# Kernel optimization log

Hardware: AMD Instinct MI355X
Metric: run time of the kernel (lower is better)

Reference implementation:

```python
import jax, jax.numpy as jnp
import numpy as np

N_GENE, N_DRUG, N_CLASS, N_FAM = 100000, 50000, 2000, 5000
D = 64
E_CG, E_CP, E_GF = 2000000, 100000, 200000
N_PAIRS = 100000


def setup_inputs() -> dict:
    key = jax.random.key(0)
    ks = jax.random.split(key, 32)
    nrm = lambda k, s, sc=0.1: jax.random.normal(k, s, jnp.float32) * sc
    ri = lambda k, n, hi: jax.random.randint(k, (n,), 0, hi, jnp.int32)
    inp = {
        "gene_emb": nrm(ks[0], (N_GENE, D)),
        "drug_emb": nrm(ks[1], (N_DRUG, D)),
        "class_emb": nrm(ks[2], (N_CLASS, D)),
        "family_emb": nrm(ks[3], (N_FAM, D)),
        "W_msg": nrm(ks[4], (2, 6, D, D)),
        "b_msg": jnp.zeros((2, 6, D), jnp.float32),
        "W_root": nrm(ks[5], (2, 6, D, D)),
        "Wc1": nrm(ks[6], (2 * D, D)),
        "bc1": jnp.zeros((D,), jnp.float32),
        "Wc2": nrm(ks[7], (D, 4)),
        "bc2": jnp.zeros((4,), jnp.float32),
        "e_cg_src": ri(ks[8], E_CG, N_DRUG), "e_cg_dst": ri(ks[9], E_CG, N_GENE),
        "e_gc_src": ri(ks[10], E_CG, N_GENE), "e_gc_dst": ri(ks[11], E_CG, N_DRUG),
        "e_cp_src": ri(ks[12], E_CP, N_DRUG), "e_cp_dst": ri(ks[13], E_CP, N_CLASS),
        "e_pc_src": ri(ks[14], E_CP, N_CLASS), "e_pc_dst": ri(ks[15], E_CP, N_DRUG),
        "e_gf_src": ri(ks[16], E_GF, N_GENE), "e_gf_dst": ri(ks[17], E_GF, N_FAM),
        "e_fg_src": ri(ks[18], E_GF, N_FAM), "e_fg_dst": ri(ks[19], E_GF, N_GENE),
        "pair_drug": ri(ks[20], N_PAIRS, N_DRUG),
        "pair_gene": ri(ks[21], N_PAIRS, N_GENE),
    }
    return inp


def _sage(x_src, x_dst, src, dst, n_dst, Wm, bm, Wr):
    # PyG SAGEConv(aggr='mean'): lin_l(mean_j x_src[j]) + lin_r(x_dst)
    msg = x_src[src]                                            # [E, D] gather
    agg = jax.ops.segment_sum(msg, dst, num_segments=n_dst)     # [n_dst, D]
    cnt = jax.ops.segment_sum(jnp.ones(src.shape, msg.dtype), dst, num_segments=n_dst)
    mean = agg / jnp.maximum(cnt, 1.0)[:, None]                 # isolated nodes -> 0
    return mean @ Wm + bm + x_dst @ Wr


def reference(gene_emb, drug_emb, class_emb, family_emb, W_msg, b_msg, W_root,
              Wc1, bc1, Wc2, bc2,
              e_cg_src, e_cg_dst, e_gc_src, e_gc_dst, e_cp_src, e_cp_dst,
              e_pc_src, e_pc_dst, e_gf_src, e_gf_dst, e_fg_src, e_fg_dst,
              pair_drug, pair_gene):
    sizes = {"gene": N_GENE, "compound": N_DRUG, "pclass": N_CLASS, "family": N_FAM}
    rels = [  # (src_type, dst_type, src_idx, dst_idx), order matches W_msg relation axis
        ("compound", "gene", e_cg_src, e_cg_dst),
        ("gene", "compound", e_gc_src, e_gc_dst),
        ("compound", "pclass", e_cp_src, e_cp_dst),
        ("pclass", "compound", e_pc_src, e_pc_dst),
        ("gene", "family", e_gf_src, e_gf_dst),
        ("family", "gene", e_fg_src, e_fg_dst),
    ]
    x = {"gene": gene_emb, "compound": drug_emb, "pclass": class_emb, "family": family_emb}
    num_layers = 2
    for l in range(num_layers):
        out = {k: jnp.zeros((sizes[k], D), jnp.float32) for k in sizes}  # HeteroConv aggr='sum'
        for r, (s, d, src, dst) in enumerate(rels):
            out[d] = out[d] + _sage(x[s], x[d], src, dst, sizes[d],
                                    W_msg[l, r], b_msg[l, r], W_root[l, r])
        x = out
        if l < num_layers - 1:
            x = {k: jax.nn.relu(v) for k, v in x.items()}  # dropout = identity (eval)
    h = jnp.concatenate([x["compound"][pair_drug], x["gene"][pair_gene]], axis=-1)  # [N, 2D]
    h = jax.nn.relu(h @ Wc1 + bc1)
    return h @ Wc2 + bc2  # [N, 4]
```

## Files before the change

kernel.cpp:

```cpp
#include <hip/hip_runtime.h>
#include <hip/hip_bf16.h>

#define NG 100000
#define ND 50000
#define NC 2000
#define NF 5000
#define DD 64

#define BSH 9
#define BINW 512
#define NREL 6
#define NB_CG ((NG + BINW - 1) / BINW)
#define NB_GC ((ND + BINW - 1) / BINW)
#define NB_CP ((NC + BINW - 1) / BINW)
#define NB_PC ((ND + BINW - 1) / BINW)
#define NB_GF ((NF + BINW - 1) / BINW)
#define NB_FG ((NG + BINW - 1) / BINW)
#define TOTB (NB_CG + NB_GC + NB_CP + NB_PC + NB_GF + NB_FG)
#define CHUNK 4096

typedef _Float16 h2_t __attribute__((ext_vector_type(2)));
typedef _Float16 half8 __attribute__((ext_vector_type(8)));
typedef float f32x4 __attribute__((ext_vector_type(4)));

__device__ inline uint packh2_rne(float a, float b) {
    h2_t h; h.x = (_Float16)a; h.y = (_Float16)b;
    return __builtin_bit_cast(uint, h);
}
__device__ inline float2 h2f2(uint u) {
    h2_t h = __builtin_bit_cast(h2_t, u);
    return make_float2((float)h.x, (float)h.y);
}
__device__ inline float fdot2u(uint m, uint w, float acc) {
#if __has_builtin(__builtin_amdgcn_fdot2)
    return __builtin_amdgcn_fdot2(__builtin_bit_cast(h2_t, m),
                                  __builtin_bit_cast(h2_t, w), acc, false);
#else
    float2 a = h2f2(m), b = h2f2(w);
    return acc + a.x * b.x + a.y * b.y;
#endif
}

struct Cvt4 { const float* in[4]; uint* out[4]; int n2[4]; };
struct EdgeJobs {
    const int* src[NREL]; const int* dst[NREL];
    int binbase[NREL]; int E[NREL]; int blk_end[NREL];
};
struct BPackJobs {
    const float* A[6]; const float* B[6]; const float* Ra[6]; const float* Rb[6];
    uint4* out[6]; int nkt[6];
};

struct MegaA {
    EdgeJobs ej; Cvt4 cv; BPackJobs bp;
    const float* Wc1; uint2* pwWc1;
    int hist_blocks, cvt_blocks;
    int* ghist;
};
__global__ __launch_bounds__(256) void megaA_kernel(MegaA a) {
    int b = blockIdx.x;
    if (b < a.hist_blocks) {
        __shared__ int lh[TOTB];
        for (int t = threadIdx.x; t < TOTB; t += 256) lh[t] = 0;
        __syncthreads();
        int j = 0;
        while (b >= a.ej.blk_end[j]) ++j;
        int b0 = j ? a.ej.blk_end[j - 1] : 0;
        int e0 = (b - b0) * CHUNK;
        const int* dst = a.ej.dst[j];
        int E = a.ej.E[j], bb = a.ej.binbase[j];
        for (int t = threadIdx.x; t < CHUNK; t += 256) {
            int e = e0 + t;
            if (e < E) atomicAdd(&lh[bb + (dst[e] >> BSH)], 1);
        }
        __syncthreads();
        for (int t = threadIdx.x; t < TOTB; t += 256)
            if (lh[t]) atomicAdd(&a.ghist[t], lh[t]);
    } else if (b < a.hist_blocks + a.cvt_blocks) {
        int cb = b - a.hist_blocks;
        for (int j = 0; j < 4; ++j) {
            int n2 = a.cv.n2[j];
            const float2* ip = (const float2*)a.cv.in[j];
            uint* op = a.cv.out[j];
            for (int i = cb * 256 + threadIdx.x; i < n2; i += a.cvt_blocks * 256)
                op[i] = packh2_rne(ip[i].x, ip[i].y);
        }
    } else if (b == a.hist_blocks + a.cvt_blocks) {
        const float* A = a.Wc1;
        uint2* o = a.pwWc1;
        for (int t = threadIdx.x; t < 32 * 64; t += 256) {
            int k4 = t >> 6, c = t & 63;
            float v0 = A[(4 * k4 + 0) * 64 + c];
            float v1 = A[(4 * k4 + 1) * 64 + c];
            float v2 = A[(4 * k4 + 2) * 64 + c];
            float v3 = A[(4 * k4 + 3) * 64 + c];
            o[t] = make_uint2(packh2_rne(v0, v1), packh2_rne(v2, v3));
        }
    } else {
        int pj = b - a.hist_blocks - a.cvt_blocks - 1;
        const float* A = a.bp.A[pj];
        const float* B = a.bp.B[pj];
        const float* Ra = a.bp.Ra[pj];
        const float* Rb = a.bp.Rb[pj];
        uint4* o = a.bp.out[pj];
        int n = a.bp.nkt[pj] * 4 * 64;
        for (int t = threadIdx.x; t < n; t += 256) {
            int kt = t >> 8, nt = (t >> 6) & 3, l = t & 63;
            int col = nt * 16 + (l & 15);
            float v[8];
#pragma unroll
            for (int j = 0; j < 8; ++j) {
                int k = kt * 32 + ((l >> 4) << 3) + j;
                int sel = k >> 6, r = k & 63;
                float x;
                if (sel == 0) x = A[r * 64 + col];
                else if (sel == 1 && B) x = B[r * 64 + col];
                else x = Ra[r * 64 + col] + (Rb ? Rb[r * 64 + col] : 0.f);
                v[j] = x;
            }
            o[t] = make_uint4(packh2_rne(v[0], v[1]), packh2_rne(v[2], v[3]),
                              packh2_rne(v[4], v[5]), packh2_rne(v[6], v[7]));
        }
    }
}

__global__ void scanB_kernel(const int* __restrict__ ghist, int* __restrict__ gbinstart,
                             int* __restrict__ gcursor) {
    int lane = threadIdx.x;
    if (lane >= 64) return;
    int carry = 0;
    for (int base = 0; base < TOTB; base += 64) {
        int idx = base + lane;
        int v = (idx < TOTB) ? ghist[idx] : 0;
        int ts = v;
        for (int d = 1; d < 64; d <<= 1) { int t = __shfl_up(ts, d); if (lane >= d) ts += t; }
        int excl = carry + ts - v;
        if (idx < TOTB) { gbinstart[idx] = excl; gcursor[idx] = excl; }
        carry += __shfl(ts, 63);
    }
    if (lane == 0) gbinstart[TOTB] = carry;
}

__global__ __launch_bounds__(256) void scatC_kernel(EdgeJobs ej, int* __restrict__ gcursor,
                                                    int* __restrict__ binned) {
    __shared__ int lh[TOTB], lbase[TOTB];
    for (int t = threadIdx.x; t < TOTB; t += 256) lh[t] = 0;
    __syncthreads();
    int b = blockIdx.x, j = 0;
    while (b >= ej.blk_end[j]) ++j;
    int b0 = j ? ej.blk_end[j - 1] : 0;
    int e0 = (b - b0) * CHUNK;
    const int* dst = ej.dst[j];
    const int* srcp = ej.src[j];
    int E = ej.E[j], bb = ej.binbase[j];
    for (int t = threadIdx.x; t < CHUNK; t += 256) {
        int e = e0 + t;
        if (e < E) atomicAdd(&lh[bb + (dst[e] >> BSH)], 1);
    }
    __syncthreads();
    for (int t = threadIdx.x; t < TOTB; t += 256) {
        int c = lh[t];
        if (c) { lbase[t] = atomicAdd(&gcursor[t], c); lh[t] = 0; }
    }
    __syncthreads();
    for (int t = threadIdx.x; t < CHUNK; t += 256) {
        int e = e0 + t;
        if (e < E) {
            int d = dst[e];
            int bin = bb + (d >> BSH);
            int p = atomicAdd(&lh[bin], 1);
            binned[lbase[bin] + p] = (srcp[e] << BSH) | (d & (BINW - 1));
        }
    }
}

struct BinMeta { int relbase[NREL + 1]; int* off[NREL]; int ndst[NREL]; };
__global__ __launch_bounds__(256) void csrD_kernel(BinMeta bmt, const int* __restrict__ gbinstart,
                                                   const int* __restrict__ binned,
                                                   int* __restrict__ adj) {
    __shared__ int lcnt[BINW], lexc[BINW];
    int b = blockIdx.x, j = 0;
    while (b >= bmt.relbase[j + 1]) ++j;
    int lb = b - bmt.relbase[j];
    int n0 = lb << BSH;
    int nn = bmt.ndst[j] - n0; if (nn > BINW) nn = BINW;
    int es = gbinstart[b], ee = gbinstart[b + 1];
    for (int t = threadIdx.x; t < BINW; t += 256) lcnt[t] = 0;
    __syncthreads();
    for (int t = es + threadIdx.x; t < ee; t += 256)
        atomicAdd(&lcnt[binned[t] & (BINW - 1)], 1);
    __syncthreads();
    if (threadIdx.x < 64) {
        int lane = threadIdx.x, carry = 0;
        for (int base = 0; base < BINW; base += 64) {
            int v = lcnt[base + lane];
            int ts = v;
            for (int d = 1; d < 64; d <<= 1) { int t2 = __shfl_up(ts, d); if (lane >= d) ts += t2; }
            lexc[base + lane] = carry + ts - v;
            carry += __shfl(ts, 63);
        }
    }
    __syncthreads();
    int* off = bmt.off[j];
    for (int t = threadIdx.x; t < nn; t += 256) off[n0 + t] = es + lexc[t];
    if (threadIdx.x == 0 && n0 + nn == bmt.ndst[j]) off[bmt.ndst[j]] = ee;
    for (int t = threadIdx.x; t < BINW; t += 256) lcnt[t] = 0;
    __syncthreads();
    for (int t = es + threadIdx.x; t < ee; t += 256) {
        int v = binned[t];
        int dl = v & (BINW - 1);
        int p = atomicAdd(&lcnt[dl], 1);
        adj[es + lexc[dl] + p] = v >> BSH;
    }
}

struct GJob { const int* off; const uint4* x; uint4* cat; int cstr, colbase, n, mode; };
struct GatherJobs { GJob jb[6]; int blk_end[6]; };

__global__ __launch_bounds__(256) void gather_kernel(GatherJobs g, const int* __restrict__ adj) {
    int b = blockIdx.x, j = 0;
    while (b >= g.blk_end[j]) ++j;
    int b0 = j ? g.blk_end[j - 1] : 0;
    int nbk = g.blk_end[j] - b0;
    GJob jb = g.jb[j];
    int tid = threadIdx.x, w = tid >> 6, lane = tid & 63;
    int cq = lane & 7, rg = lane >> 3;
    if (jb.mode == 0) {
        int side = rg >> 2, sub = rg & 3;
        int npair = (jb.n + 1) >> 1;
        for (int p = (b - b0) * 4 + w; p < npair; p += nbk * 4) {
            int ia = p * 2;
            bool hb = (ia + 1 < jb.n);
            int a0 = jb.off[ia], a1 = jb.off[ia + 1];
            int b1 = hb ? jb.off[ia + 2] : a1;
            int cnt = side ? (b1 - a1) : (a1 - a0);
            const int* base = adj + (side ? a1 : a0);
            half8 acc = {0, 0, 0, 0, 0, 0, 0, 0};
            int full = cnt & ~3;
            for (int e = sub; e < full; e += 4) {
                int idx = base[e];
                acc += *(const half8*)(jb.x + (long long)idx * 8 + cq);
            }
            int e = full + sub;
            if (e < cnt) {
                int idx = base[e];
                acc += *(const half8*)(jb.x + (long long)idx * 8 + cq);
            }
            uint4 u = __builtin_bit_cast(uint4, acc), o;
            o.x = __shfl_xor((int)u.x, 8); o.y = __shfl_xor((int)u.y, 8);
            o.z = __shfl_xor((int)u.z, 8); o.w = __shfl_xor((int)u.w, 8);
            acc += __builtin_bit_cast(half8, o);
            u = __builtin_bit_cast(uint4, acc);
            o.x = __shfl_xor((int)u.x, 16); o.y = __shfl_xor((int)u.y, 16);
            o.z = __shfl_xor((int)u.z, 16); o.w = __shfl_xor((int)u.w, 16);
            acc += __builtin_bit_cast(half8, o);
            float invf = 1.f / fmaxf((float)cnt, 1.f);
            _Float16 ih = (_Float16)invf;
            half8 iv = {ih, ih, ih, ih, ih, ih, ih, ih};
            acc *= iv;
            if (sub == 0 && (side == 0 || hb)) {
                int node = ia + side;
                jb.cat[(long long)node * jb.cstr + jb.colbase + cq] =
                    __builtin_bit_cast(uint4, acc);
            }
        }
    } else {
        for (int gp = (b - b0) * 4 + w; gp * 8 < jb.n; gp += nbk * 4) {
            int node = gp * 8 + rg;
            int nc = node < jb.n ? node : jb.n - 1;
            int o0 = jb.off[nc], o1 = jb.off[nc + 1];
            int cnt = (node < jb.n) ? (o1 - o0) : 0;
            half8 acc = {0, 0, 0, 0, 0, 0, 0, 0};
            for (int t = 0; t < cnt; ++t) {
                int idx = adj[o0 + t];
                acc += *(const half8*)(jb.x + (long long)idx * 8 + cq);
            }
            float invf = 1.f / fmaxf((float)cnt, 1.f);
            _Float16 ih = (_Float16)invf;
            half8 iv = {ih, ih, ih, ih, ih, ih, ih, ih};
            acc *= iv;
            if (node < jb.n)
                jb.cat[(long long)node * jb.cstr + jb.colbase + cq] =
                    __builtin_bit_cast(uint4, acc);
        }
    }
}

struct ApplyJobs {
    const uint4* cat[4]; const uint4* xr[4]; const uint4* Bimg[4];
    const float* bA[4]; const float* bB[4];
    ushort* out[4];
    int cat_kt[4]; int cstr4[4]; int n[4]; int relu[4]; int blk_end[4];
};
__global__ __launch_bounds__(256) void apply_kernel(ApplyJobs a, int njobs) {
    int b = blockIdx.x, j = 0;
    while (b >= a.blk_end[j]) ++j;
    int b0 = j ? a.blk_end[j - 1] : 0;
    int jb = a.blk_end[j] - b0;
    int n = a.n[j], cat_kt = a.cat_kt[j], cstr4 = a.cstr4[j], relu = a.relu[j];
    int K_kt = cat_kt + 2;
    const uint4* cat = a.cat[j];
    const uint4* xr = a.xr[j];
    const uint4* Bimg = a.Bimg[j];
    const float* bA = a.bA[j];
    const float* bB = a.bB[j];
    ushort* out = a.out[j];
    int tid = threadIdx.x;
    int w = tid >> 6, lane = tid & 63;
    int mrow = lane & 15, koct = lane >> 4;
    int tiles = (n + 15) >> 4;
    for (int t = (b - b0) * 4 + w; t < tiles; t += jb * 4) {
        int m0 = t << 4;
        int row = m0 + mrow;
        if (row > n - 1) row = n - 1;
        f32x4 acc0 = {0.f, 0.f, 0.f, 0.f};
        f32x4 acc1 = {0.f, 0.f, 0.f, 0.f};
        f32x4 acc2 = {0.f, 0.f, 0.f, 0.f};
        f32x4 acc3 = {0.f, 0.f, 0.f, 0.f};
        for (int kt = 0; kt < K_kt; ++kt) {
            uint4 av;
            if (kt < cat_kt) av = cat[(long long)row * cstr4 + kt * 4 + koct];
            else av = xr[(long long)row * 8 + (kt - cat_kt) * 4 + koct];
            half8 af = __builtin_bit_cast(half8, av);
            const uint4* bp = Bimg + kt * 256 + lane;
            half8 b0f = __builtin_bit_cast(half8, bp[0]);
            half8 b1f = __builtin_bit_cast(half8, bp[64]);
            half8 b2f = __builtin_bit_cast(half8, bp[128]);
            half8 b3f = __builtin_bit_cast(half8, bp[192]);
            acc0 = __builtin_amdgcn_mfma_f32_16x16x32_f16(af, b0f, acc0, 0, 0, 0);
            acc1 = __builtin_amdgcn_mfma_f32_16x16x32_f16(af, b1f, acc1, 0, 0, 0);
            acc2 = __builtin_amdgcn_mfma_f32_16x16x32_f16(af, b2f, acc2, 0, 0, 0);
            acc3 = __builtin_amdgcn_mfma_f32_16x16x32_f16(af, b3f, acc3, 0, 0, 0);
        }
        int c = lane & 15, r0 = m0 + (lane >> 4) * 4;
        f32x4 accs[4] = {acc0, acc1, acc2, acc3};
#pragma unroll
        for (int nt = 0; nt < 4; ++nt) {
            int col = nt * 16 + c;
            float bias = bA[col] + (bB ? bB[col] : 0.f);
#pragma unroll
            for (int r = 0; r < 4; ++r) {
                int rw = r0 + r;
                if (rw < n) {
                    float v = accs[nt][r] + bias;
                    if (relu) v = fmaxf(v, 0.f);
                    out[(long long)rw * 64 + col] = __builtin_bit_cast(ushort, (_Float16)v);
                }
            }
        }
    }
}

__global__ __launch_bounds__(256) void classifier_kernel(
        const ushort* __restrict__ xc, const ushort* __restrict__ xg,
        const int* __restrict__ pd, const int* __restrict__ pg,
        const uint2* __restrict__ gW1, const float* __restrict__ bc1,
        const float* __restrict__ Wc2, const float* __restrict__ bc2,
        float* __restrict__ out, int n) {
    __shared__ uint2 sW1[2048];
    __shared__ float sW2[256];
    __shared__ uint2 shp[4][32];
    __shared__ float sh1[4][65];
    int tid = threadIdx.x;
    for (int t = tid; t < 2048; t += 256) sW1[t] = gW1[t];
    if (tid < 256) sW2[tid] = Wc2[tid];
    __syncthreads();
    int lane = tid & 63, sub = tid >> 6;
    float b1 = bc1[lane];
    const uint* xcp = (const uint*)xc;
    const uint* xgp = (const uint*)xg;
    for (int base = blockIdx.x * 4; base < n; base += gridDim.x * 4) {
        int p = base + sub;
        if (p >= n) continue;
        int dp = pd[p], gp = pg[p];
        uint v = (lane < 32) ? xcp[(long long)dp * 32 + lane]
                             : xgp[(long long)gp * 32 + (lane - 32)];
        ((uint*)&shp[sub][0])[lane] = v;
        float acc = b1;
#pragma unroll
        for (int k4 = 0; k4 < 32; ++k4) {
            uint2 wv = sW1[k4 * 64 + lane];
            uint2 mv = shp[sub][k4];
            acc = fdot2u(mv.x, wv.x, acc);
            acc = fdot2u(mv.y, wv.y, acc);
        }
        sh1[sub][lane] = fmaxf(acc, 0.f);
        if (lane < 4) {
            float a2 = bc2[lane];
#pragma unroll 16
            for (int k = 0; k < 64; ++k) a2 += sh1[sub][k] * sW2[k * 4 + lane];
            out[(long long)p * 4 + lane] = a2;
        }
    }
}

extern "C" void kernel_launch(void* const* d_in, const int* in_sizes, int n_in,
                              void* d_out, int out_size, void* d_ws, size_t ws_size,
                              hipStream_t stream) {
    const float* gene = (const float*)d_in[0];
    const float* drug = (const float*)d_in[1];
    const float* pcls = (const float*)d_in[2];
    const float* famb = (const float*)d_in[3];
    const float* Wm   = (const float*)d_in[4];
    const float* bm   = (const float*)d_in[5];
    const float* Wr   = (const float*)d_in[6];
    const float* Wc1  = (const float*)d_in[7];
    const float* bc1  = (const float*)d_in[8];
    const float* Wc2  = (const float*)d_in[9];
    const float* bc2  = (const float*)d_in[10];
    const int* ecg_s = (const int*)d_in[11];
    const int* ecg_d = (const int*)d_in[12];
    const int* egc_s = (const int*)d_in[13];
    const int* egc_d = (const int*)d_in[14];
    const int* ecp_s = (const int*)d_in[15];
    const int* ecp_d = (const int*)d_in[16];
    const int* epc_s = (const int*)d_in[17];
    const int* epc_d = (const int*)d_in[18];
    const int* egf_s = (const int*)d_in[19];
    const int* egf_d = (const int*)d_in[20];
    const int* efg_s = (const int*)d_in[21];
    const int* efg_d = (const int*)d_in[22];
    const int* pair_d = (const int*)d_in[23];
    const int* pair_g = (const int*)d_in[24];
    const int E_CG = in_sizes[11];
    const int E_CP = in_sizes[15];
    const int E_GF = in_sizes[19];
    const int N_PAIRS = in_sizes[23];
    const long long TOT_E = 2LL * E_CG + 2LL * E_CP + 2LL * E_GF;

    ushort* g16   = (ushort*)d_ws;
    ushort* d16   = g16   + (long long)NG * DD;
    ushort* p16   = d16   + (long long)ND * DD;
    ushort* f16b  = p16   + (long long)NC * DD;
    ushort* x1g16 = f16b  + (long long)NF * DD;
    ushort* x1c16 = x1g16 + (long long)NG * DD;
    ushort* x1p16 = x1c16 + (long long)ND * DD;
    ushort* x1f16 = x1p16 + (long long)NC * DD;
    ushort* x2g16 = g16;
    ushort* x2c16 = d16;
    uint2* pwWc1 = (uint2*)(x1f16 + (long long)NF * DD);
    uint4* bimg = (uint4*)(pwWc1 + 2048);
    int* ghist = (int*)(bimg + 6 * 1536);
    int* gbinstart = ghist + TOTB;
    int* gcursor = gbinstart + TOTB + 1;
    int* off_cg = gcursor + TOTB;
    int* off_gc = off_cg + NG + 1;
    int* off_cp = off_gc + ND + 1;
    int* off_pc = off_cp + NC + 1;
    int* off_gf = off_pc + ND + 1;
    int* off_fg = off_gf + NF + 1;
    long long binned_off = (long long)(off_fg + NG + 1 - (int*)d_ws);
    binned_off = (binned_off + 3) & ~3LL;
    int* binned = (int*)d_ws + binned_off;
    int* adj    = binned + TOT_E;
    uint4* cat_c = (uint4*)binned;
    uint4* cat_p = cat_c + (long long)ND * 16;
    uint4* cat_f = cat_p + (long long)NC * 8;
    uint4* cat_g = (uint4*)(adj + TOT_E);

    auto WmLR = [&](int l, int r) { return Wm + (long long)(l * 6 + r) * DD * DD; };
    auto WrLR = [&](int l, int r) { return Wr + (long long)(l * 6 + r) * DD * DD; };
    auto bmLR = [&](int l, int r) { return bm + (long long)(l * 6 + r) * DD; };

    EdgeJobs ej;
    const int* srcs[NREL] = {ecg_s, egc_s, ecp_s, epc_s, egf_s, efg_s};
    const int* dsts[NREL] = {ecg_d, egc_d, ecp_d, epc_d, egf_d, efg_d};
    int Es[NREL] = {E_CG, E_CG, E_CP, E_CP, E_GF, E_GF};
    int bb[NREL] = {0, NB_CG, NB_CG + NB_GC, NB_CG + NB_GC + NB_CP,
                    NB_CG + NB_GC + NB_CP + NB_PC, NB_CG + NB_GC + NB_CP + NB_PC + NB_GF};
    int acc_blocks = 0;
    for (int j = 0; j < NREL; ++j) {
        ej.src[j] = srcs[j]; ej.dst[j] = dsts[j];
        ej.E[j] = Es[j]; ej.binbase[j] = bb[j];
        acc_blocks += (Es[j] + CHUNK - 1) / CHUNK;
        ej.blk_end[j] = acc_blocks;
    }
    const int THIST = acc_blocks;
    const int CVTB = 1024;

    hipMemsetAsync(ghist, 0, TOTB * sizeof(int), stream);
    MegaA ma;
    ma.ej = ej;
    ma.cv.in[0] = gene; ma.cv.out[0] = (uint*)g16;  ma.cv.n2[0] = NG * DD / 2;
    ma.cv.in[1] = drug; ma.cv.out[1] = (uint*)d16;  ma.cv.n2[1] = ND * DD / 2;
    ma.cv.in[2] = pcls; ma.cv.out[2] = (uint*)p16;  ma.cv.n2[2] = NC * DD / 2;
    ma.cv.in[3] = famb; ma.cv.out[3] = (uint*)f16b; ma.cv.n2[3] = NF * DD / 2;
    ma.Wc1 = Wc1; ma.pwWc1 = pwWc1;
    auto setbp = [&](int j, const float* A, const float* B, const float* Ra, const float* Rb, int nkt) {
        ma.bp.A[j] = A; ma.bp.B[j] = B; ma.bp.Ra[j] = Ra; ma.bp.Rb[j] = Rb;
        ma.bp.out[j] = bimg + j * 1536; ma.bp.nkt[j] = nkt;
    };
    setbp(0, WmLR(0, 0), WmLR(0, 5), WrLR(0, 0), WrLR(0, 5), 6);
    setbp(1, WmLR(0, 1), WmLR(0, 3), WrLR(0, 1), WrLR(0, 3), 6);
    setbp(2, WmLR(0, 2), nullptr,    WrLR(0, 2), nullptr,    4);
    setbp(3, WmLR(0, 4), nullptr,    WrLR(0, 4), nullptr,    4);
    setbp(4, WmLR(1, 0), WmLR(1, 5), WrLR(1, 0), WrLR(1, 5), 6);
    setbp(5, WmLR(1, 1), WmLR(1, 3), WrLR(1, 1), WrLR(1, 3), 6);
    ma.hist_blocks = THIST; ma.cvt_blocks = CVTB;
    ma.ghist = ghist;
    megaA_kernel<<<THIST + CVTB + 1 + 6, 256, 0, stream>>>(ma);

    scanB_kernel<<<1, 64, 0, stream>>>(ghist, gbinstart, gcursor);
    scatC_kernel<<<THIST, 256, 0, stream>>>(ej, gcursor, binned);
    BinMeta bmt;
    int rb[NREL + 1] = {0, NB_CG, NB_CG + NB_GC, NB_CG + NB_GC + NB_CP,
                        NB_CG + NB_GC + NB_CP + NB_PC,
                        NB_CG + NB_GC + NB_CP + NB_PC + NB_GF, TOTB};
    int* offs[NREL] = {off_cg, off_gc, off_cp, off_pc, off_gf, off_fg};
    int nds[NREL] = {NG, ND, NC, ND, NF, NG};
    for (int j = 0; j <= NREL; ++j) bmt.relbase[j] = rb[j];
    for (int j = 0; j < NREL; ++j) { bmt.off[j] = offs[j]; bmt.ndst[j] = nds[j]; }
    csrD_kernel<<<TOTB, 256, 0, stream>>>(bmt, gbinstart, binned, adj);

    auto ablk = [](int n) { int b = ((n + 15) / 16 + 3) / 4; return b > 1024 ? 1024 : b; };
    auto gb = [](int E) { int b = E / 1024; if (b < 8) b = 8; if (b > 2048) b = 2048; return b; };

    {
        GatherJobs g;
        int acc = 0;
        auto setg = [&](int j, const int* off, const ushort* x, uint4* cat,
                        int cstr, int colbase, int n, int mode, int E) {
            g.jb[j].off = off; g.jb[j].x = (const uint4*)x; g.jb[j].cat = cat;
            g.jb[j].cstr = cstr; g.jb[j].colbase = colbase; g.jb[j].n = n; g.jb[j].mode = mode;
            acc += gb(E); g.blk_end[j] = acc;
        };
        setg(0, off_cg, d16,  cat_g, 16, 0, NG, 0, E_CG);
        setg(1, off_fg, f16b, cat_g, 16, 8, NG, 1, E_GF);
        setg(2, off_gc, g16,  cat_c, 16, 0, ND, 0, E_CG);
        setg(3, off_pc, p16,  cat_c, 16, 8, ND, 1, E_CP);
        setg(4, off_cp, d16,  cat_p, 8, 0, NC, 0, E_CP);
        setg(5, off_gf, g16,  cat_f, 8, 0, NF, 0, E_GF);
        gather_kernel<<<acc, 256, 0, stream>>>(g, adj);

        ApplyJobs ap;
        auto seta = [&](int j, const uint4* cat, int ckt, int cstr4, const ushort* xr,
                        const uint4* Bi, const float* biA, const float* biB,
                        ushort* out, int n, int relu) {
            ap.cat[j] = cat; ap.cat_kt[j] = ckt; ap.cstr4[j] = cstr4;
            ap.xr[j] = (const uint4*)xr; ap.Bimg[j] = Bi; ap.bA[j] = biA; ap.bB[j] = biB;
            ap.out[j] = out; ap.n[j] = n; ap.relu[j] = relu;
        };
        seta(0, cat_g, 4, 16, g16,  bimg + 0 * 1536, bmLR(0, 0), bmLR(0, 5), x1g16, NG, 1);
        seta(1, cat_c, 4, 16, d16,  bimg + 1 * 1536, bmLR(0, 1), bmLR(0, 3), x1c16, ND, 1);
        seta(2, cat_p, 2, 8,  p16,  bimg + 2 * 1536, bmLR(0, 2), nullptr,    x1p16, NC, 1);
        seta(3, cat_f, 2, 8,  f16b, bimg + 3 * 1536, bmLR(0, 4), nullptr,    x1f16, NF, 1);
        int acc2 = 0;
        for (int j = 0; j < 4; ++j) { acc2 += ablk(ap.n[j]); ap.blk_end[j] = acc2; }
        apply_kernel<<<acc2, 256, 0, stream>>>(ap, 4);
    }

    {
        GatherJobs g;
        int acc = 0;
        auto setg = [&](int j, const int* off, const ushort* x, uint4* cat,
                        int cstr, int colbase, int n, int mode, int E) {
            g.jb[j].off = off; g.jb[j].x = (const uint4*)x; g.jb[j].cat = cat;
            g.jb[j].cstr = cstr; g.jb[j].colbase = colbase; g.jb[j].n = n; g.jb[j].mode = mode;
            acc += gb(E); g.blk_end[j] = acc;
        };
        setg(0, off_cg, x1c16, cat_g, 16, 0, NG, 0, E_CG);
        setg(1, off_fg, x1f16, cat_g, 16, 8, NG, 1, E_GF);
        setg(2, off_gc, x1g16, cat_c, 16, 0, ND, 0, E_CG);
        setg(3, off_pc, x1p16, cat_c, 16, 8, ND, 1, E_CP);
        g.jb[4] = g.jb[3]; g.jb[4].n = 0; g.blk_end[4] = acc;
        g.jb[5] = g.jb[3]; g.jb[5].n = 0; g.blk_end[5] = acc;
        gather_kernel<<<acc, 256, 0, stream>>>(g, adj);

        ApplyJobs ap;
        ap.cat[0] = cat_g; ap.cat_kt[0] = 4; ap.cstr4[0] = 16;
        ap.xr[0] = (const uint4*)x1g16; ap.Bimg[0] = bimg + 4 * 1536;
        ap.bA[0] = bmLR(1, 0); ap.bB[0] = bmLR(1, 5);
        ap.out[0] = x2g16; ap.n[0] = NG; ap.relu[0] = 0;
        ap.cat[1] = cat_c; ap.cat_kt[1] = 4; ap.cstr4[1] = 16;
        ap.xr[1] = (const uint4*)x1c16; ap.Bimg[1] = bimg + 5 * 1536;
        ap.bA[1] = bmLR(1, 1); ap.bB[1] = bmLR(1, 3);
        ap.out[1] = x2c16; ap.n[1] = ND; ap.relu[1] = 0;
        for (int j = 2; j < 4; ++j) { ap.cat[j] = nullptr; ap.xr[j] = nullptr; ap.Bimg[j] = nullptr; ap.bA[j] = nullptr; ap.bB[j] = nullptr; ap.out[j] = nullptr; ap.n[j] = 0; ap.relu[j] = 0; ap.cat_kt[j] = 2; ap.cstr4[j] = 8; }
        int acc2 = ablk(NG); ap.blk_end[0] = acc2; acc2 += ablk(ND); ap.blk_end[1] = acc2;
        ap.blk_end[2] = acc2; ap.blk_end[3] = acc2;
        apply_kernel<<<acc2, 256, 0, stream>>>(ap, 2);
    }

    int cblocks = (N_PAIRS + 3) / 4;
    if (cblocks > 2048) cblocks = 2048;
    classifier_kernel<<<cblocks, 256, 0, stream>>>(x2c16, x2g16, pair_d, pair_g,
                                                   pwWc1, bc1, Wc2, bc2,
                                                   (float*)d_out, N_PAIRS);
}
```

Baseline: 488.4 us.

## Gather high-degree relation messages from FP8 copies of node features

Adds FP8 (e4m3) shadow copies of gene and drug features, written by the conversion stage and by the layer-1 apply kernel. The mode-0 gather, which handles the two 2M-edge relations and the compound→class and gene→family relations, now reads 8-byte FP8 rows, decodes them and accumulates in fp32 instead of reading 16-byte fp16 rows. This halves the random-access gather traffic, which is the dominant cost. In exchange it adds extra FP8 writes and decode ALU work, and it loses precision in the message features, which risks accuracy tolerance.

```diff
diff --git a/kernel.cpp b/kernel.cpp
--- a/kernel.cpp
+++ b/kernel.cpp
@@ -22,10 +22,15 @@
 typedef _Float16 h2_t __attribute__((ext_vector_type(2)));
 typedef _Float16 half8 __attribute__((ext_vector_type(8)));
 typedef float f32x4 __attribute__((ext_vector_type(4)));
+typedef float f32x2 __attribute__((ext_vector_type(2)));
+typedef unsigned char uchar;
 
 __device__ inline uint packh2_rne(float a, float b) {
     h2_t h; h.x = (_Float16)a; h.y = (_Float16)b;
     return __builtin_bit_cast(uint, h);
+}
+__device__ inline uint packh2(float a, float b) {
+    return __builtin_bit_cast(uint, __builtin_amdgcn_cvt_pkrtz(a, b));
 }
 __device__ inline float2 h2f2(uint u) {
     h2_t h = __builtin_bit_cast(h2_t, u);
@@ -41,7 +46,42 @@
 #endif
 }
 
-struct Cvt4 { const float* in[4]; uint* out[4]; int n2[4]; };
+#if __has_builtin(__builtin_amdgcn_cvt_pk_f32_fp8) && __has_builtin(__builtin_amdgcn_cvt_pk_fp8_f32)
+template <bool HI>
+__device__ inline f32x2 dec_pk8(uint u) {
+    return __builtin_amdgcn_cvt_pk_f32_fp8(u, HI);
+}
+__device__ inline uint enc2_fp8(float a, float b) {
+    return __builtin_amdgcn_cvt_pk_fp8_f32(a, b, 0u, false) & 0xffffu;
+}
+__device__ inline uint enc1_fp8(float a) {
+    return __builtin_amdgcn_cvt_pk_fp8_f32(a, a, 0u, false) & 0xffu;
+}
+#else
+template <bool HI>
+__device__ inline f32x2 dec_pk8(uint u) {
+    uint pair = HI ? (u >> 16) : (u & 0xffffu);
+    uint b0 = pair & 0xffu, b1 = (pair >> 8) & 0xffu;
+    ushort h0 = (ushort)(((b0 & 0x80u) << 8) | ((b0 & 0x7fu) << 7));
+    ushort h1 = (ushort)(((b1 & 0x80u) << 8) | ((b1 & 0x7fu) << 7));
+    f32x2 r;
+    r.x = 256.f * (float)__builtin_bit_cast(_Float16, h0);
+    r.y = 256.f * (float)__builtin_bit_cast(_Float16, h1);
+    return r;
+}
+__device__ inline uint enc1_fp8(float x) {
+    ushort h = __builtin_bit_cast(ushort, (_Float16)(x * 0.00390625f));
+    uint mag = h & 0x7fffu;
+    uint r = (mag + 0x3fu + ((mag >> 7) & 1u)) >> 7;
+    if (r > 0x7eu) r = 0x7eu;
+    return r | ((h >> 8) & 0x80u);
+}
+__device__ inline uint enc2_fp8(float a, float b) {
+    return enc1_fp8(a) | (enc1_fp8(b) << 8);
+}
+#endif
+
+struct Cvt4 { const float* in[4]; uint* out[4]; ushort* out8[4]; int n2[4]; };
 struct EdgeJobs {
     const int* src[NREL]; const int* dst[NREL];
     int binbase[NREL]; int E[NREL]; int blk_end[NREL];
@@ -82,8 +122,12 @@
             int n2 = a.cv.n2[j];
             const float2* ip = (const float2*)a.cv.in[j];
             uint* op = a.cv.out[j];
-            for (int i = cb * 256 + threadIdx.x; i < n2; i += a.cvt_blocks * 256)
-                op[i] = packh2_rne(ip[i].x, ip[i].y);
+            ushort* o8 = a.cv.out8[j];
+            for (int i = cb * 256 + threadIdx.x; i < n2; i += a.cvt_blocks * 256) {
+                float2 v = ip[i];
+                op[i] = packh2_rne(v.x, v.y);
+                if (o8) o8[i] = (ushort)enc2_fp8(v.x, v.y);
+            }
         }
     } else if (b == a.hist_blocks + a.cvt_blocks) {
         const float* A = a.Wc1;
@@ -214,7 +258,7 @@
     }
 }
 
-struct GJob { const int* off; const uint4* x; uint4* cat; int cstr, colbase, n, mode; };
+struct GJob { const int* off; const void* x; uint4* cat; int cstr, colbase, n, mode; };
 struct GatherJobs { GJob jb[6]; int blk_end[6]; };
 
 __global__ __launch_bounds__(256) void gather_kernel(GatherJobs g, const int* __restrict__ adj) {
@@ -226,6 +270,7 @@
     int tid = threadIdx.x, w = tid >> 6, lane = tid & 63;
     int cq = lane & 7, rg = lane >> 3;
     if (jb.mode == 0) {
+        const uint2* x8 = (const uint2*)jb.x;
         int side = rg >> 2, sub = rg & 3;
         int npair = (jb.n + 1) >> 1;
         for (int p = (b - b0) * 4 + w; p < npair; p += nbk * 4) {
@@ -235,36 +280,41 @@
             int b1 = hb ? jb.off[ia + 2] : a1;
             int cnt = side ? (b1 - a1) : (a1 - a0);
             const int* base = adj + (side ? a1 : a0);
-            half8 acc = {0, 0, 0, 0, 0, 0, 0, 0};
+            float s0 = 0, s1 = 0, s2 = 0, s3 = 0, s4 = 0, s5 = 0, s6 = 0, s7 = 0;
             int full = cnt & ~3;
             for (int e = sub; e < full; e += 4) {
-                int idx = base[e];
-                acc += *(const half8*)(jb.x + (long long)idx * 8 + cq);
+                uint2 v = x8[(long long)base[e] * 8 + cq];
+                f32x2 p01 = dec_pk8<false>(v.x), p23 = dec_pk8<true>(v.x);
+                f32x2 p45 = dec_pk8<false>(v.y), p67 = dec_pk8<true>(v.y);
+                s0 += p01.x; s1 += p01.y; s2 += p23.x; s3 += p23.y;
+                s4 += p45.x; s5 += p45.y; s6 += p67.x; s7 += p67.y;
             }
             int e = full + sub;
             if (e < cnt) {
-                int idx = base[e];
-                acc += *(const half8*)(jb.x + (long long)idx * 8 + cq);
+                uint2 v = x8[(long long)base[e] * 8 + cq];
+                f32x2 p01 = dec_pk8<false>(v.x), p23 = dec_pk8<true>(v.x);
+                f32x2 p45 = dec_pk8<false>(v.y), p67 = dec_pk8<true>(v.y);
+                s0 += p01.x; s1 += p01.y; s2 += p23.x; s3 += p23.y;
+                s4 += p45.x; s5 += p45.y; s6 += p67.x; s7 += p67.y;
             }
-            uint4 u = __builtin_bit_cast(uint4, acc), o;
-            o.x = __shfl_xor((int)u.x, 8); o.y = __shfl_xor((int)u.y, 8);
-            o.z = __shfl_xor((int)u.z, 8); o.w = __shfl_xor((int)u.w, 8);
-            acc += __builtin_bit_cast(half8, o);
-            u = __builtin_bit_cast(uint4, acc);
-            o.x = __shfl_xor((int)u.x, 16); o.y = __shfl_xor((int)u.y, 16);
-            o.z = __shfl_xor((int)u.z, 16); o.w = __shfl_xor((int)u.w, 16);
-            acc += __builtin_bit_cast(half8, o);
+            s0 += __shfl_xor(s0, 8);  s1 += __shfl_xor(s1, 8);
+            s2 += __shfl_xor(s2, 8);  s3 += __shfl_xor(s3, 8);
+            s4 += __shfl_xor(s4, 8);  s5 += __shfl_xor(s5, 8);
+            s6 += __shfl_xor(s6, 8);  s7 += __shfl_xor(s7, 8);
+            s0 += __shfl_xor(s0, 16); s1 += __shfl_xor(s1, 16);
+            s2 += __shfl_xor(s2, 16); s3 += __shfl_xor(s3, 16);
+            s4 += __shfl_xor(s4, 16); s5 += __shfl_xor(s5, 16);
+            s6 += __shfl_xor(s6, 16); s7 += __shfl_xor(s7, 16);
             float invf = 1.f / fmaxf((float)cnt, 1.f);
-            _Float16 ih = (_Float16)invf;
-            half8 iv = {ih, ih, ih, ih, ih, ih, ih, ih};
-            acc *= iv;
             if (sub == 0 && (side == 0 || hb)) {
                 int node = ia + side;
-                jb.cat[(long long)node * jb.cstr + jb.colbase + cq] =
-                    __builtin_bit_cast(uint4, acc);
+                uint4 o = make_uint4(packh2(s0 * invf, s1 * invf), packh2(s2 * invf, s3 * invf),
+                                     packh2(s4 * invf, s5 * invf), packh2(s6 * invf, s7 * invf));
+                jb.cat[(long long)node * jb.cstr + jb.colbase + cq] = o;
             }
         }
     } else {
+        const uint4* x16 = (const uint4*)jb.x;
         for (int gp = (b - b0) * 4 + w; gp * 8 < jb.n; gp += nbk * 4) {
             int node = gp * 8 + rg;
             int nc = node < jb.n ? node : jb.n - 1;
@@ -273,7 +323,7 @@
             half8 acc = {0, 0, 0, 0, 0, 0, 0, 0};
             for (int t = 0; t < cnt; ++t) {
                 int idx = adj[o0 + t];
-                acc += *(const half8*)(jb.x + (long long)idx * 8 + cq);
+                acc += __builtin_bit_cast(half8, x16[(long long)idx * 8 + cq]);
             }
             float invf = 1.f / fmaxf((float)cnt, 1.f);
             _Float16 ih = (_Float16)invf;
@@ -289,7 +339,7 @@
 struct ApplyJobs {
     const uint4* cat[4]; const uint4* xr[4]; const uint4* Bimg[4];
     const float* bA[4]; const float* bB[4];
-    ushort* out[4];
+    ushort* out[4]; uchar* out8[4];
     int cat_kt[4]; int cstr4[4]; int n[4]; int relu[4]; int blk_end[4];
 };
 __global__ __launch_bounds__(256) void apply_kernel(ApplyJobs a, int njobs) {
@@ -305,6 +355,7 @@
     const float* bA = a.bA[j];
     const float* bB = a.bB[j];
     ushort* out = a.out[j];
+    uchar* out8 = a.out8[j];
     int tid = threadIdx.x;
     int w = tid >> 6, lane = tid & 63;
     int mrow = lane & 15, koct = lane >> 4;
@@ -344,7 +395,9 @@
                 if (rw < n) {
                     float v = accs[nt][r] + bias;
                     if (relu) v = fmaxf(v, 0.f);
-                    out[(long long)rw * 64 + col] = __builtin_bit_cast(ushort, (_Float16)v);
+                    if (out) out[(long long)rw * 64 + col] =
+                        __builtin_bit_cast(ushort, (_Float16)v);
+                    if (out8) out8[(long long)rw * 64 + col] = (uchar)enc1_fp8(v);
                 }
             }
         }
@@ -457,6 +510,10 @@
     uint4* cat_p = cat_c + (long long)ND * 16;
     uint4* cat_f = cat_p + (long long)NC * 8;
     uint4* cat_g = (uint4*)(adj + TOT_E);
+    uchar* g8  = (uchar*)(cat_g + (long long)NG * 16);
+    uchar* d8v = g8  + (long long)NG * DD;
+    uchar* x1g8 = g8;
+    uchar* x1c8 = d8v;
 
     auto WmLR = [&](int l, int r) { return Wm + (long long)(l * 6 + r) * DD * DD; };
     auto WrLR = [&](int l, int r) { return Wr + (long long)(l * 6 + r) * DD * DD; };
@@ -478,13 +535,13 @@
     const int THIST = acc_blocks;
     const int CVTB = 1024;
 
-    hipMemsetAsync(ghist, 0, TOTB * sizeof(int), stream);
+    (void)hipMemsetAsync(ghist, 0, TOTB * sizeof(int), stream);
     MegaA ma;
     ma.ej = ej;
-    ma.cv.in[0] = gene; ma.cv.out[0] = (uint*)g16;  ma.cv.n2[0] = NG * DD / 2;
-    ma.cv.in[1] = drug; ma.cv.out[1] = (uint*)d16;  ma.cv.n2[1] = ND * DD / 2;
-    ma.cv.in[2] = pcls; ma.cv.out[2] = (uint*)p16;  ma.cv.n2[2] = NC * DD / 2;
-    ma.cv.in[3] = famb; ma.cv.out[3] = (uint*)f16b; ma.cv.n2[3] = NF * DD / 2;
+    ma.cv.in[0] = gene; ma.cv.out[0] = (uint*)g16;  ma.cv.out8[0] = (ushort*)g8;  ma.cv.n2[0] = NG * DD / 2;
+    ma.cv.in[1] = drug; ma.cv.out[1] = (uint*)d16;  ma.cv.out8[1] = (ushort*)d8v; ma.cv.n2[1] = ND * DD / 2;
+    ma.cv.in[2] = pcls; ma.cv.out[2] = (uint*)p16;  ma.cv.out8[2] = nullptr;      ma.cv.n2[2] = NC * DD / 2;
+    ma.cv.in[3] = famb; ma.cv.out[3] = (uint*)f16b; ma.cv.out8[3] = nullptr;      ma.cv.n2[3] = NF * DD / 2;
     ma.Wc1 = Wc1; ma.pwWc1 = pwWc1;
     auto setbp = [&](int j, const float* A, const float* B, const float* Ra, const float* Rb, int nkt) {
         ma.bp.A[j] = A; ma.bp.B[j] = B; ma.bp.Ra[j] = Ra; ma.bp.Rb[j] = Rb;
@@ -518,32 +575,32 @@
     {
         GatherJobs g;
         int acc = 0;
-        auto setg = [&](int j, const int* off, const ushort* x, uint4* cat,
+        auto setg = [&](int j, const int* off, const void* x, uint4* cat,
                         int cstr, int colbase, int n, int mode, int E) {
-            g.jb[j].off = off; g.jb[j].x = (const uint4*)x; g.jb[j].cat = cat;
+            g.jb[j].off = off; g.jb[j].x = x; g.jb[j].cat = cat;
             g.jb[j].cstr = cstr; g.jb[j].colbase = colbase; g.jb[j].n = n; g.jb[j].mode = mode;
             acc += gb(E); g.blk_end[j] = acc;
         };
-        setg(0, off_cg, d16,  cat_g, 16, 0, NG, 0, E_CG);
+        setg(0, off_cg, d8v,  cat_g, 16, 0, NG, 0, E_CG);
         setg(1, off_fg, f16b, cat_g, 16, 8, NG, 1, E_GF);
-        setg(2, off_gc, g16,  cat_c, 16, 0, ND, 0, E_CG);
+        setg(2, off_gc, g8,   cat_c, 16, 0, ND, 0, E_CG);
         setg(3, off_pc, p16,  cat_c, 16, 8, ND, 1, E_CP);
-        setg(4, off_cp, d16,  cat_p, 8, 0, NC, 0, E_CP);
-        setg(5, off_gf, g16,  cat_f, 8, 0, NF, 0, E_GF);
+        setg(4, off_cp, d8v,  cat_p, 8, 0, NC, 0, E_CP);
+        setg(5, off_gf, g8,   cat_f, 8, 0, NF, 0, E_GF);
         gather_kernel<<<acc, 256, 0, stream>>>(g, adj);
 
         ApplyJobs ap;
         auto seta = [&](int j, const uint4* cat, int ckt, int cstr4, const ushort* xr,
                         const uint4* Bi, const float* biA, const float* biB,
-                        ushort* out, int n, int relu) {
+                        ushort* out, uchar* out8, int n, int relu) {
             ap.cat[j] = cat; ap.cat_kt[j] = ckt; ap.cstr4[j] = cstr4;
             ap.xr[j] = (const uint4*)xr; ap.Bimg[j] = Bi; ap.bA[j] = biA; ap.bB[j] = biB;
-            ap.out[j] = out; ap.n[j] = n; ap.relu[j] = relu;
+            ap.out[j] = out; ap.out8[j] = out8; ap.n[j] = n; ap.relu[j] = relu;
         };
-        seta(0, cat_g, 4, 16, g16,  bimg + 0 * 1536, bmLR(0, 0), bmLR(0, 5), x1g16, NG, 1);
-        seta(1, cat_c, 4, 16, d16,  bimg + 1 * 1536, bmLR(0, 1), bmLR(0, 3), x1c16, ND, 1);
-        seta(2, cat_p, 2, 8,  p16,  bimg + 2 * 1536, bmLR(0, 2), nullptr,    x1p16, NC, 1);
-        seta(3, cat_f, 2, 8,  f16b, bimg + 3 * 1536, bmLR(0, 4), nullptr,    x1f16, NF, 1);
+        seta(0, cat_g, 4, 16, g16,  bimg + 0 * 1536, bmLR(0, 0), bmLR(0, 5), x1g16, x1g8, NG, 1);
+        seta(1, cat_c, 4, 16, d16,  bimg + 1 * 1536, bmLR(0, 1), bmLR(0, 3), x1c16, x1c8, ND, 1);
+        seta(2, cat_p, 2, 8,  p16,  bimg + 2 * 1536, bmLR(0, 2), nullptr,    x1p16, nullptr, NC, 1);
+        seta(3, cat_f, 2, 8,  f16b, bimg + 3 * 1536, bmLR(0, 4), nullptr,    x1f16, nullptr, NF, 1);
         int acc2 = 0;
         for (int j = 0; j < 4; ++j) { acc2 += ablk(ap.n[j]); ap.blk_end[j] = acc2; }
         apply_kernel<<<acc2, 256, 0, stream>>>(ap, 4);
@@ -552,15 +609,15 @@
     {
         GatherJobs g;
         int acc = 0;
-        auto setg = [&](int j, const int* off, const ushort* x, uint4* cat,
+        auto setg = [&](int j, const int* off, const void* x, uint4* cat,
                         int cstr, int colbase, int n, int mode, int E) {
-            g.jb[j].off = off; g.jb[j].x = (const uint4*)x; g.jb[j].cat = cat;
+            g.jb[j].off = off; g.jb[j].x = x; g.jb[j].cat = cat;
             g.jb[j].cstr = cstr; g.jb[j].colbase = colbase; g.jb[j].n = n; g.jb[j].mode = mode;
             acc += gb(E); g.blk_end[j] = acc;
         };
-        setg(0, off_cg, x1c16, cat_g, 16, 0, NG, 0, E_CG);
+        setg(0, off_cg, x1c8,  cat_g, 16, 0, NG, 0, E_CG);
         setg(1, off_fg, x1f16, cat_g, 16, 8, NG, 1, E_GF);
-        setg(2, off_gc, x1g16, cat_c, 16, 0, ND, 0, E_CG);
+        setg(2, off_gc, x1g8,  cat_c, 16, 0, ND, 0, E_CG);
         setg(3, off_pc, x1p16, cat_c, 16, 8, ND, 1, E_CP);
         g.jb[4] = g.jb[3]; g.jb[4].n = 0; g.blk_end[4] = acc;
         g.jb[5] = g.jb[3]; g.jb[5].n = 0; g.blk_end[5] = acc;
@@ -570,12 +627,16 @@
         ap.cat[0] = cat_g; ap.cat_kt[0] = 4; ap.cstr4[0] = 16;
         ap.xr[0] = (const uint4*)x1g16; ap.Bimg[0] = bimg + 4 * 1536;
         ap.bA[0] = bmLR(1, 0); ap.bB[0] = bmLR(1, 5);
-        ap.out[0] = x2g16; ap.n[0] = NG; ap.relu[0] = 0;
+        ap.out[0] = x2g16; ap.out8[0] = nullptr; ap.n[0] = NG; ap.relu[0] = 0;
         ap.cat[1] = cat_c; ap.cat_kt[1] = 4; ap.cstr4[1] = 16;
         ap.xr[1] = (const uint4*)x1c16; ap.Bimg[1] = bimg + 5 * 1536;
         ap.bA[1] = bmLR(1, 1); ap.bB[1] = bmLR(1, 3);
-        ap.out[1] = x2c16; ap.n[1] = ND; ap.relu[1] = 0;
-        for (int j = 2; j < 4; ++j) { ap.cat[j] = nullptr; ap.xr[j] = nullptr; ap.Bimg[j] = nullptr; ap.bA[j] = nullptr; ap.bB[j] = nullptr; ap.out[j] = nullptr; ap.n[j] = 0; ap.relu[j] = 0; ap.cat_kt[j] = 2; ap.cstr4[j] = 8; }
+        ap.out[1] = x2c16; ap.out8[1] = nullptr; ap.n[1] = ND; ap.relu[1] = 0;
+        for (int j = 2; j < 4; ++j) {
+            ap.cat[j] = nullptr; ap.xr[j] = nullptr; ap.Bimg[j] = nullptr;
+            ap.bA[j] = nullptr; ap.bB[j] = nullptr; ap.out[j] = nullptr; ap.out8[j] = nullptr;
+            ap.n[j] = 0; ap.relu[j] = 0; ap.cat_kt[j] = 2; ap.cstr4[j] = 8;
+        }
         int acc2 = ablk(NG); ap.blk_end[0] = acc2; acc2 += ablk(ND); ap.blk_end[1] = acc2;
         ap.blk_end[2] = acc2; ap.blk_end[3] = acc2;
         apply_kernel<<<acc2, 256, 0, stream>>>(ap, 2);
```

Measured after the change: 486.0 us. About the same (-0.5%).
